# Kernel optimization log

Measured on AMD Instinct MI355X. Metric: run time of the kernel, lower is better.

The kernel has to match this reference:

```python
import jax, jax.numpy as jnp
import numpy as np

B, T, C = 4, 2048, 1024
H = 16
D = C // H  # head_size = 64


def setup_inputs() -> dict:
    key = jax.random.key(0)
    k1, k2, k3 = jax.random.split(key, 3)
    x = jax.random.normal(k1, (B, T, C), dtype=jnp.float32)
    # weights stored pre-transposed relative to torch nn.Linear: y = x @ w
    w_attn = jax.random.normal(k2, (C, 3 * C), dtype=jnp.float32) * (1.0 / np.sqrt(C))
    w_proj = jax.random.normal(k3, (C, C), dtype=jnp.float32) * (1.0 / np.sqrt(C))
    return {"x": x, "w_attn": w_attn, "w_proj": w_proj}


def reference(x, w_attn, w_proj):
    # Dropout layers are identity in eval mode (reference baseline).
    Bx, Tx, Cx = x.shape
    qkv = x @ w_attn                                   # [B,T,3C]
    q, k, v = jnp.split(qkv, 3, axis=2)
    # [B,T,C] -> [B,H,T,D]
    def heads(t):
        return t.reshape(Bx, Tx, H, D).transpose(0, 2, 1, 3)
    q, k, v = heads(q), heads(k), heads(v)
    scale = 1.0 / np.sqrt(D).astype(np.float32)
    att = jnp.einsum('bhqd,bhkd->bhqk', q, k) * scale   # [B,H,T,T]
    causal = jnp.tril(jnp.ones((Tx, Tx), dtype=bool))
    att = jnp.where(causal[None, None], att, -jnp.inf)
    att = jax.nn.softmax(att, axis=-1)
    y = jnp.einsum('bhqk,bhkd->bhqd', att, v)           # [B,H,T,D]
    y = y.transpose(0, 2, 1, 3).reshape(Bx, Tx, Cx)     # [B,T,C]
    return y @ w_proj
```

## Files before the change

kernel.cpp:

```cpp
#include <hip/hip_runtime.h>

typedef unsigned short ushort;
typedef short short8 __attribute__((ext_vector_type(8)));
typedef short short4v __attribute__((ext_vector_type(4)));
typedef float f32x4 __attribute__((ext_vector_type(4)));
typedef __attribute__((address_space(3))) unsigned int lds_u32;
typedef __attribute__((address_space(1))) const unsigned int glb_u32;

#define DEVI static __device__ __forceinline__

DEVI ushort f2b(float f) {
  union { float f; unsigned u; } x; x.f = f;
  unsigned r = x.u + 0x7fffu + ((x.u >> 16) & 1u);
  return (ushort)(r >> 16);
}

DEVI void gload_lds16(const ushort* g, ushort* l) {
  __builtin_amdgcn_global_load_lds((glb_u32*)g, (lds_u32*)l, 16, 0, 0);
}

__global__ __launch_bounds__(256) void prep_kernel(
    const float* __restrict__ x, const float* __restrict__ wa,
    const float* __restrict__ wp, ushort* __restrict__ xb,
    ushort* __restrict__ watT, ushort* __restrict__ wpT) {
  __shared__ float tile[32][33];
  const int bid = blockIdx.x, tid = threadIdx.x;
  if (bid < 4096) {
    int i = bid * 256 + tid;
    const float4* p = (const float4*)x + 2 * (size_t)i;
    float4 a = p[0], b = p[1];
    ushort tmp[8] = { f2b(a.x), f2b(a.y), f2b(a.z), f2b(a.w),
                      f2b(b.x), f2b(b.y), f2b(b.z), f2b(b.w) };
    *(short8*)(xb + 8 * (size_t)i) = *(short8*)tmp;
    return;
  }
  const float* in; ushort* out; int R, C, bx, by;
  if (bid < 7168) {
    int bb = bid - 4096; in = wa; out = watT; R = 1024; C = 3072;
    bx = (bb % 96) * 32; by = (bb / 96) * 32;
  } else {
    int bb = bid - 7168; in = wp; out = wpT; R = 1024; C = 1024;
    bx = (bb % 32) * 32; by = (bb / 32) * 32;
  }
  const int tx = tid & 31, ty = tid >> 5;
#pragma unroll
  for (int i = 0; i < 32; i += 8)
    tile[ty + i][tx] = in[(size_t)(by + ty + i) * C + bx + tx];
  __syncthreads();
#pragma unroll
  for (int i = 0; i < 32; i += 8)
    out[(size_t)(bx + ty + i) * R + by + tx] = f2b(tile[tx][ty + i]);
}

template <bool OUT_F32, bool QKV>
__global__ __launch_bounds__(256) void gemm_bt_kernel(
    const ushort* __restrict__ A, const ushort* __restrict__ BT,
    void* __restrict__ C_, ushort* __restrict__ vt, int M, int N, int K) {
  __shared__ ushort lA[128 * 32];
  __shared__ ushort lB[128 * 32];
  const int tid = threadIdx.x, lane = tid & 63, wave = tid >> 6;
  const int wr = wave >> 1, wc = wave & 1;
  const int m0 = blockIdx.x * 128, n0 = blockIdx.y * 128;
  const int g = lane >> 4, c = lane & 15;
  f32x4 acc[4][4] = {};
  for (int kt = 0; kt < K; kt += 32) {
    __syncthreads();
#pragma unroll
    for (int it = 0; it < 2; ++it) {
      int idx = it * 256 + tid;
      int row = idx >> 2, ch = idx & 3;
      gload_lds16(A + (size_t)(m0 + row) * K + kt + ch * 8,
                  lA + (size_t)(it * 256 + wave * 64) * 8);
      gload_lds16(BT + (size_t)(n0 + row) * K + kt + ch * 8,
                  lB + (size_t)(it * 256 + wave * 64) * 8);
    }
    __syncthreads();
    short8 af[4], bf[4];
#pragma unroll
    for (int mi = 0; mi < 4; ++mi)
      af[mi] = *(const short8*)&lA[(wr * 64 + mi * 16 + c) * 32 + g * 8];
#pragma unroll
    for (int ni = 0; ni < 4; ++ni)
      bf[ni] = *(const short8*)&lB[(wc * 64 + ni * 16 + c) * 32 + g * 8];
#pragma unroll
    for (int mi = 0; mi < 4; ++mi)
#pragma unroll
      for (int ni = 0; ni < 4; ++ni)
        acc[mi][ni] = __builtin_amdgcn_mfma_f32_16x16x32_bf16(af[mi], bf[ni], acc[mi][ni], 0, 0, 0);
  }
  if (QKV && n0 >= 2048) {
#pragma unroll
    for (int mi = 0; mi < 4; ++mi)
#pragma unroll
      for (int ni = 0; ni < 4; ++ni) {
        int mrow0 = m0 + wr * 64 + mi * 16 + g * 4;
        int ncol = n0 - 2048 + wc * 64 + ni * 16 + c;
        int b = mrow0 >> 11, t0 = mrow0 & 2047;
        int hh = ncol >> 6, d = ncol & 63;
        ushort tmp[4] = { f2b(acc[mi][ni][0]), f2b(acc[mi][ni][1]),
                          f2b(acc[mi][ni][2]), f2b(acc[mi][ni][3]) };
        *(short4v*)&vt[((size_t)(b * 16 + hh) * 64 + d) * 2048 + t0] = *(short4v*)tmp;
      }
    return;
  }
#pragma unroll
  for (int mi = 0; mi < 4; ++mi)
#pragma unroll
    for (int ni = 0; ni < 4; ++ni)
#pragma unroll
      for (int r = 0; r < 4; ++r) {
        int mrow = m0 + wr * 64 + mi * 16 + g * 4 + r;
        int ncol = n0 + wc * 64 + ni * 16 + c;
        if (OUT_F32) ((float*)C_)[(size_t)mrow * N + ncol] = acc[mi][ni][r];
        else         ((ushort*)C_)[(size_t)mrow * N + ncol] = f2b(acc[mi][ni][r]);
      }
}

DEVI void attn_compute(const short8 (&qf)[2], f32x4 (&o)[4], float (&l)[4],
                       int qb_t, int kv, const ushort* __restrict__ kb,
                       const ushort* __restrict__ vb, ushort* __restrict__ pW,
                       int wave, int g, int c, int e) {
  const float C1 = 0.18033688011112042f;
  const float SH = 17.312340490667562f;
  f32x4 s[4];
#pragma unroll
  for (int n = 0; n < 4; ++n) {
    short8 kf0 = *(const short8*)&kb[(n * 16 + c) * 64 + ((g ^ e) * 8)];
    short8 kf1 = *(const short8*)&kb[(n * 16 + c) * 64 + (((4 + g) ^ e) * 8)];
    s[n] = (f32x4){0.f, 0.f, 0.f, 0.f};
    s[n] = __builtin_amdgcn_mfma_f32_16x16x32_bf16(qf[0], kf0, s[n], 0, 0, 0);
    s[n] = __builtin_amdgcn_mfma_f32_16x16x32_bf16(qf[1], kf1, s[n], 0, 0, 0);
  }
  if (kv == qb_t) {
#pragma unroll
    for (int n = 0; n < 4; ++n)
#pragma unroll
      for (int r = 0; r < 4; ++r)
        if ((n * 16 + c) > (wave * 16 + g * 4 + r)) s[n][r] = -INFINITY;
  }
#pragma unroll
  for (int n = 0; n < 4; ++n)
#pragma unroll
    for (int r = 0; r < 4; ++r) {
      float p = __builtin_amdgcn_exp2f(fmaf(s[n][r], C1, -SH));
      l[r] += p;
      union { float f; unsigned u; } pu; pu.f = p;
      int row = g * 4 + r;
      pW[row * 64 + (((n * 2 + (c >> 3)) ^ (row & 7)) * 8) + (c & 7)] =
          (ushort)((pu.u + 0x8000u) >> 16);
    }
  short8 pf0 = *(const short8*)&pW[c * 64 + ((g ^ e) * 8)];
  short8 pf1 = *(const short8*)&pW[c * 64 + (((4 + g) ^ e) * 8)];
#pragma unroll
  for (int dg = 0; dg < 4; ++dg) {
    short8 vf0 = *(const short8*)&vb[(dg * 16 + c) * 64 + ((g ^ e) * 8)];
    short8 vf1 = *(const short8*)&vb[(dg * 16 + c) * 64 + (((4 + g) ^ e) * 8)];
    o[dg] = __builtin_amdgcn_mfma_f32_16x16x32_bf16(pf0, vf0, o[dg], 0, 0, 0);
    o[dg] = __builtin_amdgcn_mfma_f32_16x16x32_bf16(pf1, vf1, o[dg], 0, 0, 0);
  }
}

DEVI void attn_store(const f32x4 (&o)[4], float (&l)[4], ushort* __restrict__ y,
                     int b, int h, int qb_t, int wave, int g, int c) {
#pragma unroll
  for (int r = 0; r < 4; ++r) {
    float s0 = l[r];
    s0 += __shfl_xor(s0, 1);
    s0 += __shfl_xor(s0, 2);
    s0 += __shfl_xor(s0, 4);
    s0 += __shfl_xor(s0, 8);
    l[r] = 1.0f / s0;
  }
#pragma unroll
  for (int dg = 0; dg < 4; ++dg)
#pragma unroll
    for (int r = 0; r < 4; ++r) {
      size_t row = (size_t)b * 2048 + qb_t * 64 + wave * 16 + g * 4 + r;
      y[row * 1024 + h * 64 + dg * 16 + c] = f2b(o[dg][r] * l[r]);
    }
}

__global__ __launch_bounds__(256, 2) void attn_kernel(
    const ushort* __restrict__ qkv, const ushort* __restrict__ vt,
    ushort* __restrict__ y) {
  __shared__ ushort kT[64 * 64];
  __shared__ ushort vT[64 * 64];
  __shared__ ushort pB[4][16 * 64];
  const int tid = threadIdx.x, lane = tid & 63, wave = tid >> 6;
  const int g = lane >> 4, c = lane & 15, e = c & 7;
  const int j = blockIdx.x, bh = blockIdx.y;
  const int b = bh >> 4, h = bh & 15;
  const int qb0 = j, qb1 = 31 - j;
  const size_t base = (size_t)b * 2048 * 3072 + (size_t)h * 64;
  const ushort* qp = qkv + base;
  const ushort* kp = qkv + base + 1024;
  const ushort* vp = vt + (size_t)bh * 64 * 2048;

  short8 qf0[2], qf1[2];
  {
    int qrow0 = qb0 * 64 + wave * 16 + c;
    int qrow1 = qb1 * 64 + wave * 16 + c;
    qf0[0] = *(const short8*)(qp + (size_t)qrow0 * 3072 + g * 8);
    qf0[1] = *(const short8*)(qp + (size_t)qrow0 * 3072 + 32 + g * 8);
    qf1[0] = *(const short8*)(qp + (size_t)qrow1 * 3072 + g * 8);
    qf1[1] = *(const short8*)(qp + (size_t)qrow1 * 3072 + 32 + g * 8);
  }
  f32x4 o0[4] = {}, o1[4] = {};
  float l0[4] = {0.f, 0.f, 0.f, 0.f}, l1[4] = {0.f, 0.f, 0.f, 0.f};

  auto stage = [&](int kv) {
#pragma unroll
    for (int it = 0; it < 2; ++it) {
      int idx = it * 256 + tid;
      int row = idx >> 3, ch = idx & 7;
      int chs = ch ^ (row & 7);
      gload_lds16(kp + (size_t)(kv * 64 + row) * 3072 + chs * 8, kT + idx * 8);
      gload_lds16(vp + (size_t)row * 2048 + kv * 64 + chs * 8, vT + idx * 8);
    }
  };

  for (int kv = 0; kv <= qb1; ++kv) {
    stage(kv);
    asm volatile("s_waitcnt vmcnt(0)" ::: "memory");
    __builtin_amdgcn_s_barrier();
    __builtin_amdgcn_sched_barrier(0);
    attn_compute(qf1, o1, l1, qb1, kv, kT, vT, pB[wave], wave, g, c, e);
    if (kv <= qb0)
      attn_compute(qf0, o0, l0, qb0, kv, kT, vT, pB[wave], wave, g, c, e);
    __builtin_amdgcn_s_barrier();
  }

  attn_store(o0, l0, y, b, h, qb0, wave, g, c);
  attn_store(o1, l1, y, b, h, qb1, wave, g, c);
}

extern "C" void kernel_launch(void* const* d_in, const int* in_sizes, int n_in,
                              void* d_out, int out_size, void* d_ws, size_t ws_size,
                              hipStream_t stream) {
  const float* x      = (const float*)d_in[0];
  const float* w_attn = (const float*)d_in[1];
  const float* w_proj = (const float*)d_in[2];
  float* out = (float*)d_out;

  ushort* xb   = (ushort*)d_ws;
  ushort* watT = xb   + (size_t)8192 * 1024;
  ushort* wpT  = watT + (size_t)3072 * 1024;
  ushort* qkvb = wpT  + (size_t)1024 * 1024;
  ushort* yb   = qkvb + (size_t)8192 * 3072;
  ushort* vtb  = yb   + (size_t)8192 * 1024;

  prep_kernel<<<8192, 256, 0, stream>>>(x, w_attn, w_proj, xb, watT, wpT);
  gemm_bt_kernel<false, true><<<dim3(64, 24), 256, 0, stream>>>(
      xb, watT, qkvb, vtb, 8192, 3072, 1024);
  attn_kernel<<<dim3(16, 64), 256, 0, stream>>>(qkvb, vtb, yb);
  gemm_bt_kernel<true, false><<<dim3(64, 8), 256, 0, stream>>>(
      yb, wpT, out, nullptr, 8192, 1024, 1024);
}
```

Measured before the change: 192.6 us.

## Rewrite GEMM with 256x128 tiles, double-buffered LDS, swizzle, and block remap

Replaces the single-buffered 128x128 GEMM with a 512-thread kernel on 256x128 tiles and K-steps of 64. Global-to-LDS loads are double-buffered with partial vmcnt waits so the next tile loads while MFMAs run. LDS chunks are XOR-swizzled to avoid bank conflicts, workgroup IDs are remapped for better L2 locality, and MFMA sections are wrapped in setprio. LDS use grows to 96KB per block, which may limit occupancy.

```diff
diff --git a/kernel.cpp b/kernel.cpp
--- a/kernel.cpp
+++ b/kernel.cpp
@@ -53,48 +53,83 @@
 }
 
 template <bool OUT_F32, bool QKV>
-__global__ __launch_bounds__(256) void gemm_bt_kernel(
+__global__ __launch_bounds__(512) void gemm2_kernel(
     const ushort* __restrict__ A, const ushort* __restrict__ BT,
     void* __restrict__ C_, ushort* __restrict__ vt, int M, int N, int K) {
-  __shared__ ushort lA[128 * 32];
-  __shared__ ushort lB[128 * 32];
+  __shared__ ushort lA[2][256 * 64];
+  __shared__ ushort lB[2][128 * 64];
   const int tid = threadIdx.x, lane = tid & 63, wave = tid >> 6;
-  const int wr = wave >> 1, wc = wave & 1;
-  const int m0 = blockIdx.x * 128, n0 = blockIdx.y * 128;
+  const int wr = wave >> 2, wc = wave & 3;
   const int g = lane >> 4, c = lane & 15;
-  f32x4 acc[4][4] = {};
-  for (int kt = 0; kt < K; kt += 32) {
-    __syncthreads();
+  const int nx = gridDim.x, nwg = nx * gridDim.y;
+  int lin = blockIdx.y * nx + blockIdx.x;
+  lin = (lin & 7) * (nwg >> 3) + (lin >> 3);
+  const int m0 = (lin % nx) * 256, n0 = (lin / nx) * 128;
+
+  auto stage = [&](int t, int buf) {
+    const int kt = t << 6;
+#pragma unroll
+    for (int it = 0; it < 4; ++it) {
+      int idx = it * 512 + tid;
+      int row = idx >> 3, ch = idx & 7;
+      int chs = ch ^ (row & 7);
+      gload_lds16(A + (size_t)(m0 + row) * K + kt + chs * 8, lA[buf] + idx * 8);
+    }
 #pragma unroll
     for (int it = 0; it < 2; ++it) {
-      int idx = it * 256 + tid;
-      int row = idx >> 2, ch = idx & 3;
-      gload_lds16(A + (size_t)(m0 + row) * K + kt + ch * 8,
-                  lA + (size_t)(it * 256 + wave * 64) * 8);
-      gload_lds16(BT + (size_t)(n0 + row) * K + kt + ch * 8,
-                  lB + (size_t)(it * 256 + wave * 64) * 8);
-    }
-    __syncthreads();
-    short8 af[4], bf[4];
-#pragma unroll
-    for (int mi = 0; mi < 4; ++mi)
-      af[mi] = *(const short8*)&lA[(wr * 64 + mi * 16 + c) * 32 + g * 8];
-#pragma unroll
-    for (int ni = 0; ni < 4; ++ni)
-      bf[ni] = *(const short8*)&lB[(wc * 64 + ni * 16 + c) * 32 + g * 8];
-#pragma unroll
-    for (int mi = 0; mi < 4; ++mi)
-#pragma unroll
-      for (int ni = 0; ni < 4; ++ni)
-        acc[mi][ni] = __builtin_amdgcn_mfma_f32_16x16x32_bf16(af[mi], bf[ni], acc[mi][ni], 0, 0, 0);
-  }
+      int idx = it * 512 + tid;
+      int row = idx >> 3, ch = idx & 7;
+      int chs = ch ^ (row & 7);
+      gload_lds16(BT + (size_t)(n0 + row) * K + kt + chs * 8, lB[buf] + idx * 8);
+    }
+  };
+
+  f32x4 acc[8][2] = {};
+  const int nt = K >> 6;
+  stage(0, 0);
+  for (int t = 0; t < nt; ++t) {
+    const int cur = t & 1;
+    if (t + 1 < nt) {
+      stage(t + 1, cur ^ 1);
+      asm volatile("s_waitcnt vmcnt(6)" ::: "memory");
+    } else {
+      asm volatile("s_waitcnt vmcnt(0)" ::: "memory");
+    }
+    __builtin_amdgcn_s_barrier();
+    __builtin_amdgcn_sched_barrier(0);
+    const ushort* a_ = lA[cur];
+    const ushort* b_ = lB[cur];
+    short8 bf[2][2];
+#pragma unroll
+    for (int ni = 0; ni < 2; ++ni) {
+      int rb = wc * 32 + ni * 16 + c;
+#pragma unroll
+      for (int ks = 0; ks < 2; ++ks)
+        bf[ni][ks] = *(const short8*)&b_[rb * 64 + (((ks * 4 + g) ^ (rb & 7)) * 8)];
+    }
+#pragma unroll
+    for (int mi = 0; mi < 8; ++mi) {
+      int ra = wr * 128 + mi * 16 + c;
+      short8 af0 = *(const short8*)&a_[ra * 64 + ((g ^ (ra & 7)) * 8)];
+      short8 af1 = *(const short8*)&a_[ra * 64 + (((4 + g) ^ (ra & 7)) * 8)];
+      __builtin_amdgcn_s_setprio(1);
+#pragma unroll
+      for (int ni = 0; ni < 2; ++ni) {
+        acc[mi][ni] = __builtin_amdgcn_mfma_f32_16x16x32_bf16(af0, bf[ni][0], acc[mi][ni], 0, 0, 0);
+        acc[mi][ni] = __builtin_amdgcn_mfma_f32_16x16x32_bf16(af1, bf[ni][1], acc[mi][ni], 0, 0, 0);
+      }
+      __builtin_amdgcn_s_setprio(0);
+    }
+    __builtin_amdgcn_s_barrier();
+  }
+
   if (QKV && n0 >= 2048) {
 #pragma unroll
-    for (int mi = 0; mi < 4; ++mi)
-#pragma unroll
-      for (int ni = 0; ni < 4; ++ni) {
-        int mrow0 = m0 + wr * 64 + mi * 16 + g * 4;
-        int ncol = n0 - 2048 + wc * 64 + ni * 16 + c;
+    for (int mi = 0; mi < 8; ++mi)
+#pragma unroll
+      for (int ni = 0; ni < 2; ++ni) {
+        int mrow0 = m0 + wr * 128 + mi * 16 + g * 4;
+        int ncol = n0 - 2048 + wc * 32 + ni * 16 + c;
         int b = mrow0 >> 11, t0 = mrow0 & 2047;
         int hh = ncol >> 6, d = ncol & 63;
         ushort tmp[4] = { f2b(acc[mi][ni][0]), f2b(acc[mi][ni][1]),
@@ -104,13 +139,13 @@
     return;
   }
 #pragma unroll
-  for (int mi = 0; mi < 4; ++mi)
-#pragma unroll
-    for (int ni = 0; ni < 4; ++ni)
+  for (int mi = 0; mi < 8; ++mi)
+#pragma unroll
+    for (int ni = 0; ni < 2; ++ni)
 #pragma unroll
       for (int r = 0; r < 4; ++r) {
-        int mrow = m0 + wr * 64 + mi * 16 + g * 4 + r;
-        int ncol = n0 + wc * 64 + ni * 16 + c;
+        int mrow = m0 + wr * 128 + mi * 16 + g * 4 + r;
+        int ncol = n0 + wc * 32 + ni * 16 + c;
         if (OUT_F32) ((float*)C_)[(size_t)mrow * N + ncol] = acc[mi][ni][r];
         else         ((ushort*)C_)[(size_t)mrow * N + ncol] = f2b(acc[mi][ni][r]);
       }
@@ -250,9 +285,9 @@
   ushort* vtb  = yb   + (size_t)8192 * 1024;
 
   prep_kernel<<<8192, 256, 0, stream>>>(x, w_attn, w_proj, xb, watT, wpT);
-  gemm_bt_kernel<false, true><<<dim3(64, 24), 256, 0, stream>>>(
+  gemm2_kernel<false, true><<<dim3(32, 24), 512, 0, stream>>>(
       xb, watT, qkvb, vtb, 8192, 3072, 1024);
   attn_kernel<<<dim3(16, 64), 256, 0, stream>>>(qkvb, vtb, yb);
-  gemm_bt_kernel<true, false><<<dim3(64, 8), 256, 0, stream>>>(
+  gemm2_kernel<true, false><<<dim3(32, 8), 512, 0, stream>>>(
       yb, wpT, out, nullptr, 8192, 1024, 1024);
 }
```

After: 212.1 us. 1.1x slower.

## Prefetch next K/V tile into registers while computing current attention tile

Applied to the files above, without the earlier changes.

Replaces the synchronous global-to-LDS direct loads of K and V with a register-staged software pipeline. The next tile's loads are issued into registers before the compute on the current tile and written to LDS at the top of the following iteration. This hides global-load latency behind the QK/PV compute, in exchange for extra VGPRs and explicit LDS store instructions instead of the direct load path.

```diff
diff --git a/kernel.cpp b/kernel.cpp
--- a/kernel.cpp
+++ b/kernel.cpp
@@ -208,26 +208,33 @@
   f32x4 o0[4] = {}, o1[4] = {};
   float l0[4] = {0.f, 0.f, 0.f, 0.f}, l1[4] = {0.f, 0.f, 0.f, 0.f};
 
-  auto stage = [&](int kv) {
-#pragma unroll
-    for (int it = 0; it < 2; ++it) {
-      int idx = it * 256 + tid;
-      int row = idx >> 3, ch = idx & 7;
-      int chs = ch ^ (row & 7);
-      gload_lds16(kp + (size_t)(kv * 64 + row) * 3072 + chs * 8, kT + idx * 8);
-      gload_lds16(vp + (size_t)row * 2048 + kv * 64 + chs * 8, vT + idx * 8);
-    }
+  short8 kr0, kr1, vr0, vr1;
+  const int row0 = tid >> 3, ch0 = tid & 7;
+  const int row1 = (256 + tid) >> 3, ch1 = tid & 7;
+  const int cs0 = ch0 ^ (row0 & 7), cs1 = ch1 ^ (row1 & 7);
+
+  auto issue = [&](int kv) {
+    kr0 = *(const short8*)(kp + (size_t)(kv * 64 + row0) * 3072 + cs0 * 8);
+    kr1 = *(const short8*)(kp + (size_t)(kv * 64 + row1) * 3072 + cs1 * 8);
+    vr0 = *(const short8*)(vp + (size_t)row0 * 2048 + kv * 64 + cs0 * 8);
+    vr1 = *(const short8*)(vp + (size_t)row1 * 2048 + kv * 64 + cs1 * 8);
   };
-
+  auto commit = [&]() {
+    *(short8*)&kT[tid * 8] = kr0;
+    *(short8*)&kT[(256 + tid) * 8] = kr1;
+    *(short8*)&vT[tid * 8] = vr0;
+    *(short8*)&vT[(256 + tid) * 8] = vr1;
+  };
+
+  issue(0);
   for (int kv = 0; kv <= qb1; ++kv) {
-    stage(kv);
-    asm volatile("s_waitcnt vmcnt(0)" ::: "memory");
-    __builtin_amdgcn_s_barrier();
-    __builtin_amdgcn_sched_barrier(0);
+    commit();
+    __syncthreads();
+    if (kv < qb1) issue(kv + 1);
     attn_compute(qf1, o1, l1, qb1, kv, kT, vT, pB[wave], wave, g, c, e);
     if (kv <= qb0)
       attn_compute(qf0, o0, l0, qb0, kv, kT, vT, pB[wave], wave, g, c, e);
-    __builtin_amdgcn_s_barrier();
+    __syncthreads();
   }
 
   attn_store(o0, l0, y, b, h, qb0, wave, g, c);
```

Measured after the change: 186.7 us. 3.1% less time.
